# Optimization experiments

Measured on AMD Instinct MI355X. Metric: run time of the kernel, lower is better.

The kernel has to match this reference:

```python
import jax, jax.numpy as jnp
import numpy as np

N_NODES = 100000  # static segment count for segment_sum
DEGREE = 2        # polynomial degree of the Laplacian filter


def setup_inputs() -> dict:
    key = jax.random.key(0)
    k1, k2, k3, k4 = jax.random.split(key, 4)
    N, E, C = N_NODES, 1600000, 32
    x = jax.random.normal(k1, (N, C), dtype=jnp.float32)
    weights = jax.random.normal(k2, (1 + DEGREE,), dtype=jnp.float32)
    edge_src = jax.random.randint(k3, (E,), 0, N, dtype=jnp.int32)
    edge_dst = jax.random.randint(k4, (E,), 0, N, dtype=jnp.int32)
    return {"x": x, "weights": weights, "edge_src": edge_src, "edge_dst": edge_dst}


def reference(x, weights, edge_src, edge_dst):
    """y = (w0 * I + w1 * L + ... + w_d * L^d) @ x with L = D - A,
    computed by the recurrence t_k = L @ t_{k-1} (never materializing L^k)."""
    N = N_NODES
    # node degrees: D[i] = number of edges landing on i
    deg = jax.ops.segment_sum(jnp.ones_like(edge_src, dtype=x.dtype), edge_dst,
                              num_segments=N)  # [N]

    def lap_matvec(t):
        # (L @ t)[i] = deg[i] * t[i] - sum_{(s->i) in E} t[s]
        agg = jax.ops.segment_sum(t[edge_src], edge_dst, num_segments=N)  # [N, C]
        return deg[:, None] * t - agg

    y = weights[0] * x
    t = x
    for k in range(1, 1 + DEGREE):  # fixed small loop over polynomial order
        t = lap_matvec(t)
        y = y + weights[k] * t
    return y
```

## Files before the change

kernel.cpp:

```cpp
#include <hip/hip_runtime.h>

#define C 32
#define NT 256
#define BSH 8
#define BNODE 256
#define CAPC 5632
#define SRCMASK 0x1FFFF

typedef float f32x4 __attribute__((ext_vector_type(4)));

__device__ __forceinline__ unsigned int f2bf(float f) {
    unsigned int u = __float_as_uint(f);
    return (u + 0x7FFFu + ((u >> 16) & 1u)) >> 16;
}
__device__ __forceinline__ float bflo(unsigned int u) { return __uint_as_float(u << 16); }
__device__ __forceinline__ float bfhi(unsigned int u) { return __uint_as_float(u & 0xFFFF0000u); }

__global__ __launch_bounds__(1024) void phaseA(const int* __restrict__ src,
                                               const int* __restrict__ dst,
                                               int* __restrict__ cursor,
                                               int* __restrict__ pk,
                                               int E, int nbuck, int chunk) {
    extern __shared__ int l[];
    int* lcnt = l;
    int* lcur = l + nbuck;
    int tid = threadIdx.x;
    for (int i = tid; i < nbuck; i += 1024) lcnt[i] = 0;
    __syncthreads();
    int base = blockIdx.x * chunk;
    int end  = min(base + chunk, E);
    for (int e = base + tid; e < end; e += 1024)
        atomicAdd(&lcnt[dst[e] >> BSH], 1);
    __syncthreads();
    for (int i = tid; i < nbuck; i += 1024) {
        int c = lcnt[i];
        lcur[i] = i * CAPC + (c ? atomicAdd(&cursor[i], c) : 0);
    }
    __syncthreads();
    for (int e = base + tid; e < end; e += 1024) {
        int d = dst[e];
        int b = d >> BSH;
        int pos = atomicAdd(&lcur[b], 1);
        pk[pos] = src[e] | ((d & (BNODE - 1)) << 17);
    }
}

__global__ __launch_bounds__(1024) void phaseB(int* __restrict__ pk,
                                               const int* __restrict__ cursor,
                                               int* __restrict__ row_start,
                                               int* __restrict__ ideg,
                                               const float* __restrict__ x,
                                               uint2* __restrict__ xb2, int N) {
    __shared__ int ent[CAPC];
    __shared__ int h[BNODE];
    __shared__ int ss[BNODE];
    __shared__ int cur[BNODE];
    int b = blockIdx.x;
    int tid = threadIdx.x;

    if (tid < BNODE) h[tid] = 0;

    int n0 = b << BSH;
    int nvalid = min(N - n0, BNODE);
    for (int i = tid; i < nvalid * 8; i += 1024) {
        int n = n0 + (i >> 3);
        int lq = i & 7;
        const float* xp = x + (size_t)n * C + lq * 4;
        uint2 r;
        r.x = f2bf(xp[0]) | (f2bf(xp[1]) << 16);
        r.y = f2bf(xp[2]) | (f2bf(xp[3]) << 16);
        xb2[(size_t)n * 8 + lq] = r;
    }

    int base = b * CAPC;
    int cnt = min(cursor[b], CAPC);
    __syncthreads();
    for (int i = tid; i < cnt; i += 1024) {
        int en = pk[base + i];
        ent[i] = en;
        atomicAdd(&h[en >> 17], 1);
    }
    __syncthreads();
    int v = 0;
    if (tid < BNODE) { v = h[tid]; ss[tid] = v; }
    __syncthreads();
    for (int off = 1; off < BNODE; off <<= 1) {
        int u = 0;
        if (tid < BNODE && tid >= off) u = ss[tid - off];
        __syncthreads();
        if (tid < BNODE) ss[tid] += u;
        __syncthreads();
    }
    if (tid < BNODE) {
        int exc = ss[tid] - v;
        int n = n0 + tid;
        if (n < N) { row_start[n] = base + exc; ideg[n] = v; }
        cur[tid] = exc;
    }
    __syncthreads();
    for (int i = tid; i < cnt; i += 1024) {
        int en = ent[i];
        int pos = atomicAdd(&cur[en >> 17], 1);
        pk[base + pos] = en & SRCMASK;
    }
}

__device__ __forceinline__ void accum_seg(const uint2* __restrict__ arr,
                                          const int* __restrict__ pk,
                                          int lo, int hi, int lq,
                                          float& a0, float& a1, float& a2, float& a3) {
#define ACC4(ux, uy) { a0 += bflo(ux); a1 += bfhi(ux); a2 += bflo(uy); a3 += bfhi(uy); }
    int j = lo;
    for (; j + 7 < hi; j += 8) {
        int s0 = __builtin_nontemporal_load(&pk[j]);
        int s1 = __builtin_nontemporal_load(&pk[j + 1]);
        int s2 = __builtin_nontemporal_load(&pk[j + 2]);
        int s3 = __builtin_nontemporal_load(&pk[j + 3]);
        int s4 = __builtin_nontemporal_load(&pk[j + 4]);
        int s5 = __builtin_nontemporal_load(&pk[j + 5]);
        int s6 = __builtin_nontemporal_load(&pk[j + 6]);
        int s7 = __builtin_nontemporal_load(&pk[j + 7]);
        uint2 u0 = arr[(size_t)s0 * 8 + lq];
        uint2 u1 = arr[(size_t)s1 * 8 + lq];
        uint2 u2 = arr[(size_t)s2 * 8 + lq];
        uint2 u3 = arr[(size_t)s3 * 8 + lq];
        uint2 u4 = arr[(size_t)s4 * 8 + lq];
        uint2 u5 = arr[(size_t)s5 * 8 + lq];
        uint2 u6 = arr[(size_t)s6 * 8 + lq];
        uint2 u7 = arr[(size_t)s7 * 8 + lq];
        ACC4(u0.x, u0.y) ACC4(u1.x, u1.y) ACC4(u2.x, u2.y) ACC4(u3.x, u3.y)
        ACC4(u4.x, u4.y) ACC4(u5.x, u5.y) ACC4(u6.x, u6.y) ACC4(u7.x, u7.y)
    }
    for (; j + 1 < hi; j += 2) {
        int s0 = __builtin_nontemporal_load(&pk[j]);
        int s1 = __builtin_nontemporal_load(&pk[j + 1]);
        uint2 u0 = arr[(size_t)s0 * 8 + lq];
        uint2 u1 = arr[(size_t)s1 * 8 + lq];
        ACC4(u0.x, u0.y) ACC4(u1.x, u1.y)
    }
    if (j < hi) {
        uint2 u0 = arr[(size_t)__builtin_nontemporal_load(&pk[j]) * 8 + lq];
        ACC4(u0.x, u0.y)
    }
#undef ACC4
}

__global__ __launch_bounds__(NT) void gather1_bf(const uint2* __restrict__ xb2,
        const int* __restrict__ pk, const int* __restrict__ row_start,
        const int* __restrict__ ideg, uint2* __restrict__ t1b2, int N) {
    int g = blockIdx.x * blockDim.x + threadIdx.x;
    int n = g >> 3;
    if (n >= N) return;
    int lq = g & 7;
    int rs = row_start[n];
    int dg = ideg[n];
    float a0 = 0.f, a1 = 0.f, a2 = 0.f, a3 = 0.f;
    accum_seg(xb2, pk, rs, rs + dg, lq, a0, a1, a2, a3);
    uint2 xs = xb2[(size_t)n * 8 + lq];
    float fdg = (float)dg;
    float t0 = fdg * bflo(xs.x) - a0;
    float t1v = fdg * bfhi(xs.x) - a1;
    float t2 = fdg * bflo(xs.y) - a2;
    float t3 = fdg * bfhi(xs.y) - a3;
    uint2 r;
    r.x = f2bf(t0) | (f2bf(t1v) << 16);
    r.y = f2bf(t2) | (f2bf(t3) << 16);
    t1b2[(size_t)n * 8 + lq] = r;
}

__global__ __launch_bounds__(NT) void gather2_bf(const uint2* __restrict__ xb2,
        const uint2* __restrict__ t1b2, const int* __restrict__ pk,
        const int* __restrict__ row_start, const int* __restrict__ ideg,
        const float* __restrict__ wts, float* __restrict__ y, int N) {
    int g = blockIdx.x * blockDim.x + threadIdx.x;
    int n = g >> 3;
    if (n >= N) return;
    int lq = g & 7;
    int rs = row_start[n];
    int dg = ideg[n];
    float a0 = 0.f, a1 = 0.f, a2 = 0.f, a3 = 0.f;
    accum_seg(t1b2, pk, rs, rs + dg, lq, a0, a1, a2, a3);
    uint2 xs = xb2[(size_t)n * 8 + lq];
    uint2 ts = t1b2[(size_t)n * 8 + lq];
    float w0 = wts[0], w1 = wts[1], w2 = wts[2];
    float fdg = (float)dg;
    float tv0 = bflo(ts.x), tv1 = bfhi(ts.x), tv2 = bflo(ts.y), tv3 = bfhi(ts.y);
    f32x4 r;
    r.x = w0 * bflo(xs.x) + w1 * tv0 + w2 * (fdg * tv0 - a0);
    r.y = w0 * bfhi(xs.x) + w1 * tv1 + w2 * (fdg * tv1 - a1);
    r.z = w0 * bflo(xs.y) + w1 * tv2 + w2 * (fdg * tv2 - a2);
    r.w = w0 * bfhi(xs.y) + w1 * tv3 + w2 * (fdg * tv3 - a3);
    size_t o = (size_t)n * C + lq * 4;
    __builtin_nontemporal_store(r, (f32x4*)(y + o));
}

__global__ __launch_bounds__(NT) void gather1_f32(const float* __restrict__ x,
        const int* __restrict__ pk, const int* __restrict__ row_start,
        const int* __restrict__ ideg, float* __restrict__ t1, int N) {
    int g = blockIdx.x * blockDim.x + threadIdx.x;
    int n = g >> 5;
    if (n >= N) return;
    int ch = g & 31;
    int rs = row_start[n], dg = ideg[n], re = rs + dg;
    float a0 = 0, a1 = 0, a2 = 0, a3 = 0;
    int j = rs;
    for (; j + 3 < re; j += 4) {
        a0 += x[(size_t)pk[j] * C + ch];     a1 += x[(size_t)pk[j + 1] * C + ch];
        a2 += x[(size_t)pk[j + 2] * C + ch]; a3 += x[(size_t)pk[j + 3] * C + ch];
    }
    for (; j < re; ++j) a0 += x[(size_t)pk[j] * C + ch];
    size_t o = (size_t)n * C + ch;
    t1[o] = (float)dg * x[o] - ((a0 + a1) + (a2 + a3));
}
__global__ __launch_bounds__(NT) void gather2_f32(const float* __restrict__ x,
        const float* __restrict__ t1, const int* __restrict__ pk,
        const int* __restrict__ row_start, const int* __restrict__ ideg,
        const float* __restrict__ wts, float* __restrict__ y, int N) {
    int g = blockIdx.x * blockDim.x + threadIdx.x;
    int n = g >> 5;
    if (n >= N) return;
    int ch = g & 31;
    int rs = row_start[n], dg = ideg[n], re = rs + dg;
    float a0 = 0, a1 = 0, a2 = 0, a3 = 0;
    int j = rs;
    for (; j + 3 < re; j += 4) {
        a0 += t1[(size_t)pk[j] * C + ch];     a1 += t1[(size_t)pk[j + 1] * C + ch];
        a2 += t1[(size_t)pk[j + 2] * C + ch]; a3 += t1[(size_t)pk[j + 3] * C + ch];
    }
    for (; j < re; ++j) a0 += t1[(size_t)pk[j] * C + ch];
    size_t o = (size_t)n * C + ch;
    float tv = t1[o];
    y[o] = wts[0] * x[o] + wts[1] * tv + wts[2] * ((float)dg * tv - ((a0 + a1) + (a2 + a3)));
}

extern "C" void kernel_launch(void* const* d_in, const int* in_sizes, int n_in,
                              void* d_out, int out_size, void* d_ws, size_t ws_size,
                              hipStream_t stream) {
    const float* x    = (const float*)d_in[0];
    const float* wts  = (const float*)d_in[1];
    const int*   esrc = (const int*)d_in[2];
    const int*   edst = (const int*)d_in[3];
    float*       y    = (float*)d_out;

    const int N = in_sizes[0] / C;
    const int E = in_sizes[2];
    const int nbuck = (N + BNODE - 1) >> BSH;
    const int nc = N * C;

    char* p = (char*)d_ws;
    auto align16 = [](size_t s) { return (s + 15) & ~(size_t)15; };
    int* cursor    = (int*)p; p += align16((size_t)nbuck * 4);
    int* row_start = (int*)p; p += align16((size_t)N * 4);
    int* ideg      = (int*)p; p += align16((size_t)N * 4);
    int* pk        = (int*)p; p += align16((size_t)nbuck * CAPC * 4);
    uint2* xb2     = (uint2*)p; p += align16((size_t)nc * 2);
    uint2* t1b2    = (uint2*)p; p += align16((size_t)nc * 2);
    float* t1      = (float*)p;
    bool bf_ok = (size_t)(p - (char*)d_ws) <= ws_size;

    hipMemsetAsync(cursor, 0, (size_t)nbuck * 4, stream);

    const int ABLK = 512;
    const int chunk = (E + ABLK - 1) / ABLK;
    const size_t lds_a = (size_t)nbuck * 2 * 4;
    phaseA<<<ABLK, 1024, lds_a, stream>>>(esrc, edst, cursor, pk, E, nbuck, chunk);
    phaseB<<<nbuck, 1024, 0, stream>>>(pk, cursor, row_start, ideg, x, xb2, N);

    if (bf_ok) {
        const int gblocks = ((size_t)N * 8 + NT - 1) / NT;
        gather1_bf<<<gblocks, NT, 0, stream>>>(xb2, pk, row_start, ideg, t1b2, N);
        gather2_bf<<<gblocks, NT, 0, stream>>>(xb2, t1b2, pk, row_start, ideg, wts, y, N);
    } else {
        const int gblocks = ((size_t)N * 32 + NT - 1) / NT;
        gather1_f32<<<gblocks, NT, 0, stream>>>(x, pk, row_start, ideg, t1, N);
        gather2_f32<<<gblocks, NT, 0, stream>>>(x, t1, pk, row_start, ideg, wts, y, N);
    }
}
```

Before: 174.7 us.

## Split bf16 feature arrays into two channel halves and gather each half separately

Stores the bf16 copies of x and t1 as two separate 16-channel planes and runs each gather pass twice, once per half. Each half-plane is 3.2 MB instead of 6.4 MB, so the random gathers are meant to fit better in cache and get a higher hit rate. The cost is reading the CSR index array twice per pass and launching more kernels, and each gathered row now covers 32 bytes instead of 64. It also switches the t1 stores to nontemporal stores.

```diff
diff --git a/kernel.cpp b/kernel.cpp
--- a/kernel.cpp
+++ b/kernel.cpp
@@ -50,7 +50,8 @@
                                                int* __restrict__ row_start,
                                                int* __restrict__ ideg,
                                                const float* __restrict__ x,
-                                               uint2* __restrict__ xb2, int N) {
+                                               uint2* __restrict__ xbh,
+                                               int N) {
     __shared__ int ent[CAPC];
     __shared__ int h[BNODE];
     __shared__ int ss[BNODE];
@@ -62,14 +63,17 @@
 
     int n0 = b << BSH;
     int nvalid = min(N - n0, BNODE);
-    for (int i = tid; i < nvalid * 8; i += 1024) {
-        int n = n0 + (i >> 3);
-        int lq = i & 7;
-        const float* xp = x + (size_t)n * C + lq * 4;
-        uint2 r;
-        r.x = f2bf(xp[0]) | (f2bf(xp[1]) << 16);
-        r.y = f2bf(xp[2]) | (f2bf(xp[3]) << 16);
-        xb2[(size_t)n * 8 + lq] = r;
+    size_t N4 = (size_t)N * 4;
+    for (int hh = 0; hh < 2; ++hh) {
+        for (int i = tid; i < nvalid * 4; i += 1024) {
+            int n = n0 + (i >> 2);
+            int lq2 = i & 3;
+            const float* xp = x + (size_t)n * C + hh * 16 + lq2 * 4;
+            uint2 r;
+            r.x = f2bf(xp[0]) | (f2bf(xp[1]) << 16);
+            r.y = f2bf(xp[2]) | (f2bf(xp[3]) << 16);
+            xbh[hh * N4 + (size_t)n * 4 + lq2] = r;
+        }
     }
 
     int base = b * CAPC;
@@ -105,10 +109,10 @@
     }
 }
 
-__device__ __forceinline__ void accum_seg(const uint2* __restrict__ arr,
-                                          const int* __restrict__ pk,
-                                          int lo, int hi, int lq,
-                                          float& a0, float& a1, float& a2, float& a3) {
+__device__ __forceinline__ void accum_half(const uint2* __restrict__ arr,
+                                           const int* __restrict__ pk,
+                                           int lo, int hi, int lq2,
+                                           float& a0, float& a1, float& a2, float& a3) {
 #define ACC4(ux, uy) { a0 += bflo(ux); a1 += bfhi(ux); a2 += bflo(uy); a3 += bfhi(uy); }
     int j = lo;
     for (; j + 7 < hi; j += 8) {
@@ -120,43 +124,43 @@
         int s5 = __builtin_nontemporal_load(&pk[j + 5]);
         int s6 = __builtin_nontemporal_load(&pk[j + 6]);
         int s7 = __builtin_nontemporal_load(&pk[j + 7]);
-        uint2 u0 = arr[(size_t)s0 * 8 + lq];
-        uint2 u1 = arr[(size_t)s1 * 8 + lq];
-        uint2 u2 = arr[(size_t)s2 * 8 + lq];
-        uint2 u3 = arr[(size_t)s3 * 8 + lq];
-        uint2 u4 = arr[(size_t)s4 * 8 + lq];
-        uint2 u5 = arr[(size_t)s5 * 8 + lq];
-        uint2 u6 = arr[(size_t)s6 * 8 + lq];
-        uint2 u7 = arr[(size_t)s7 * 8 + lq];
+        uint2 u0 = arr[(size_t)s0 * 4 + lq2];
+        uint2 u1 = arr[(size_t)s1 * 4 + lq2];
+        uint2 u2 = arr[(size_t)s2 * 4 + lq2];
+        uint2 u3 = arr[(size_t)s3 * 4 + lq2];
+        uint2 u4 = arr[(size_t)s4 * 4 + lq2];
+        uint2 u5 = arr[(size_t)s5 * 4 + lq2];
+        uint2 u6 = arr[(size_t)s6 * 4 + lq2];
+        uint2 u7 = arr[(size_t)s7 * 4 + lq2];
         ACC4(u0.x, u0.y) ACC4(u1.x, u1.y) ACC4(u2.x, u2.y) ACC4(u3.x, u3.y)
         ACC4(u4.x, u4.y) ACC4(u5.x, u5.y) ACC4(u6.x, u6.y) ACC4(u7.x, u7.y)
     }
     for (; j + 1 < hi; j += 2) {
         int s0 = __builtin_nontemporal_load(&pk[j]);
         int s1 = __builtin_nontemporal_load(&pk[j + 1]);
-        uint2 u0 = arr[(size_t)s0 * 8 + lq];
-        uint2 u1 = arr[(size_t)s1 * 8 + lq];
+        uint2 u0 = arr[(size_t)s0 * 4 + lq2];
+        uint2 u1 = arr[(size_t)s1 * 4 + lq2];
         ACC4(u0.x, u0.y) ACC4(u1.x, u1.y)
     }
     if (j < hi) {
-        uint2 u0 = arr[(size_t)__builtin_nontemporal_load(&pk[j]) * 8 + lq];
+        uint2 u0 = arr[(size_t)__builtin_nontemporal_load(&pk[j]) * 4 + lq2];
         ACC4(u0.x, u0.y)
     }
 #undef ACC4
 }
 
-__global__ __launch_bounds__(NT) void gather1_bf(const uint2* __restrict__ xb2,
+__global__ __launch_bounds__(NT) void gather1_half(const uint2* __restrict__ xh,
         const int* __restrict__ pk, const int* __restrict__ row_start,
-        const int* __restrict__ ideg, uint2* __restrict__ t1b2, int N) {
-    int g = blockIdx.x * blockDim.x + threadIdx.x;
-    int n = g >> 3;
-    if (n >= N) return;
-    int lq = g & 7;
+        const int* __restrict__ ideg, uint2* __restrict__ t1h, int N) {
+    int g = blockIdx.x * blockDim.x + threadIdx.x;
+    int n = g >> 2;
+    if (n >= N) return;
+    int lq2 = g & 3;
     int rs = row_start[n];
     int dg = ideg[n];
     float a0 = 0.f, a1 = 0.f, a2 = 0.f, a3 = 0.f;
-    accum_seg(xb2, pk, rs, rs + dg, lq, a0, a1, a2, a3);
-    uint2 xs = xb2[(size_t)n * 8 + lq];
+    accum_half(xh, pk, rs, rs + dg, lq2, a0, a1, a2, a3);
+    uint2 xs = xh[(size_t)n * 4 + lq2];
     float fdg = (float)dg;
     float t0 = fdg * bflo(xs.x) - a0;
     float t1v = fdg * bfhi(xs.x) - a1;
@@ -165,23 +169,24 @@
     uint2 r;
     r.x = f2bf(t0) | (f2bf(t1v) << 16);
     r.y = f2bf(t2) | (f2bf(t3) << 16);
-    t1b2[(size_t)n * 8 + lq] = r;
-}
-
-__global__ __launch_bounds__(NT) void gather2_bf(const uint2* __restrict__ xb2,
-        const uint2* __restrict__ t1b2, const int* __restrict__ pk,
+    __builtin_nontemporal_store(r.x, &((unsigned int*)t1h)[((size_t)n * 4 + lq2) * 2]);
+    __builtin_nontemporal_store(r.y, &((unsigned int*)t1h)[((size_t)n * 4 + lq2) * 2 + 1]);
+}
+
+__global__ __launch_bounds__(NT) void gather2_half(const uint2* __restrict__ xh,
+        const uint2* __restrict__ t1h, const int* __restrict__ pk,
         const int* __restrict__ row_start, const int* __restrict__ ideg,
-        const float* __restrict__ wts, float* __restrict__ y, int N) {
-    int g = blockIdx.x * blockDim.x + threadIdx.x;
-    int n = g >> 3;
-    if (n >= N) return;
-    int lq = g & 7;
+        const float* __restrict__ wts, float* __restrict__ y, int N, int hh) {
+    int g = blockIdx.x * blockDim.x + threadIdx.x;
+    int n = g >> 2;
+    if (n >= N) return;
+    int lq2 = g & 3;
     int rs = row_start[n];
     int dg = ideg[n];
     float a0 = 0.f, a1 = 0.f, a2 = 0.f, a3 = 0.f;
-    accum_seg(t1b2, pk, rs, rs + dg, lq, a0, a1, a2, a3);
-    uint2 xs = xb2[(size_t)n * 8 + lq];
-    uint2 ts = t1b2[(size_t)n * 8 + lq];
+    accum_half(t1h, pk, rs, rs + dg, lq2, a0, a1, a2, a3);
+    uint2 xs = xh[(size_t)n * 4 + lq2];
+    uint2 ts = t1h[(size_t)n * 4 + lq2];
     float w0 = wts[0], w1 = wts[1], w2 = wts[2];
     float fdg = (float)dg;
     float tv0 = bflo(ts.x), tv1 = bfhi(ts.x), tv2 = bflo(ts.y), tv3 = bfhi(ts.y);
@@ -190,7 +195,7 @@
     r.y = w0 * bfhi(xs.x) + w1 * tv1 + w2 * (fdg * tv1 - a1);
     r.z = w0 * bflo(xs.y) + w1 * tv2 + w2 * (fdg * tv2 - a2);
     r.w = w0 * bfhi(xs.y) + w1 * tv3 + w2 * (fdg * tv3 - a3);
-    size_t o = (size_t)n * C + lq * 4;
+    size_t o = (size_t)n * C + hh * 16 + lq2 * 4;
     __builtin_nontemporal_store(r, (f32x4*)(y + o));
 }
 
@@ -246,6 +251,7 @@
     const int E = in_sizes[2];
     const int nbuck = (N + BNODE - 1) >> BSH;
     const int nc = N * C;
+    const size_t N4 = (size_t)N * 4;
 
     char* p = (char*)d_ws;
     auto align16 = [](size_t s) { return (s + 15) & ~(size_t)15; };
@@ -253,9 +259,9 @@
     int* row_start = (int*)p; p += align16((size_t)N * 4);
     int* ideg      = (int*)p; p += align16((size_t)N * 4);
     int* pk        = (int*)p; p += align16((size_t)nbuck * CAPC * 4);
-    uint2* xb2     = (uint2*)p; p += align16((size_t)nc * 2);
-    uint2* t1b2    = (uint2*)p; p += align16((size_t)nc * 2);
-    float* t1      = (float*)p;
+    uint2* xbh     = (uint2*)p; p += align16(N4 * 2 * 8);
+    uint2* t1bh    = (uint2*)p; p += align16(N4 * 2 * 8);
+    float* t1      = (float*)p; p += align16((size_t)nc * 4);
     bool bf_ok = (size_t)(p - (char*)d_ws) <= ws_size;
 
     hipMemsetAsync(cursor, 0, (size_t)nbuck * 4, stream);
@@ -264,12 +270,14 @@
     const int chunk = (E + ABLK - 1) / ABLK;
     const size_t lds_a = (size_t)nbuck * 2 * 4;
     phaseA<<<ABLK, 1024, lds_a, stream>>>(esrc, edst, cursor, pk, E, nbuck, chunk);
-    phaseB<<<nbuck, 1024, 0, stream>>>(pk, cursor, row_start, ideg, x, xb2, N);
+    phaseB<<<nbuck, 1024, 0, stream>>>(pk, cursor, row_start, ideg, x, xbh, N);
 
     if (bf_ok) {
-        const int gblocks = ((size_t)N * 8 + NT - 1) / NT;
-        gather1_bf<<<gblocks, NT, 0, stream>>>(xb2, pk, row_start, ideg, t1b2, N);
-        gather2_bf<<<gblocks, NT, 0, stream>>>(xb2, t1b2, pk, row_start, ideg, wts, y, N);
+        const int gblocks = ((size_t)N * 4 + NT - 1) / NT;
+        gather1_half<<<gblocks, NT, 0, stream>>>(xbh,      pk, row_start, ideg, t1bh,      N);
+        gather1_half<<<gblocks, NT, 0, stream>>>(xbh + N4, pk, row_start, ideg, t1bh + N4, N);
+        gather2_half<<<gblocks, NT, 0, stream>>>(xbh,      t1bh,      pk, row_start, ideg, wts, y, N, 0);
+        gather2_half<<<gblocks, NT, 0, stream>>>(xbh + N4, t1bh + N4, pk, row_start, ideg, wts, y, N, 1);
     } else {
         const int gblocks = ((size_t)N * 32 + NT - 1) / NT;
         gather1_f32<<<gblocks, NT, 0, stream>>>(x, pk, row_start, ideg, t1, N);
```

Measured after the change: 201.4 us. 1.15x slower.

## Fuse first Laplacian matvec into bucket sort and bf16 convert into phaseA

Applied to the files above, without the earlier changes.

Moves the fp32-to-bf16 conversion of x into the edge-scatter kernel as a grid-stride tail loop. The first Laplacian pass is fused into the per-bucket sort kernel, reading sorted source indices from LDS instead of reloading pk from global memory. This drops the separate gather1 launch and one pass over the index array. In exchange, each bucket block now does the gather work with only 391 blocks of 1024 threads, which may reduce latency hiding, and the sort kernel needs extra LDS. A dead stub remains in the old phaseA.

```diff
diff --git a/kernel.cpp b/kernel.cpp
--- a/kernel.cpp
+++ b/kernel.cpp
@@ -20,7 +20,8 @@
                                                const int* __restrict__ dst,
                                                int* __restrict__ cursor,
                                                int* __restrict__ pk,
-                                               int E, int nbuck, int chunk) {
+                                               uint2* __restrict__ xb2,
+                                               int N, int E, int nbuck, int chunk) {
     extern __shared__ int l[];
     int* lcnt = l;
     int* lcur = l + nbuck;
@@ -43,37 +44,72 @@
         int pos = atomicAdd(&lcur[b], 1);
         pk[pos] = src[e] | ((d & (BNODE - 1)) << 17);
     }
-}
-
-__global__ __launch_bounds__(1024) void phaseB(int* __restrict__ pk,
-                                               const int* __restrict__ cursor,
-                                               int* __restrict__ row_start,
-                                               int* __restrict__ ideg,
-                                               const float* __restrict__ x,
-                                               uint2* __restrict__ xb2, int N) {
+    if (xb2 != nullptr) {
+        const float* xf = (const float*)dst;
+    }
+}
+
+__global__ __launch_bounds__(1024) void phaseA_cvt(const int* __restrict__ src,
+                                                   const int* __restrict__ dst,
+                                                   int* __restrict__ cursor,
+                                                   int* __restrict__ pk,
+                                                   const float* __restrict__ x,
+                                                   uint2* __restrict__ xb2,
+                                                   int N, int E, int nbuck, int chunk) {
+    extern __shared__ int l[];
+    int* lcnt = l;
+    int* lcur = l + nbuck;
+    int tid = threadIdx.x;
+    for (int i = tid; i < nbuck; i += 1024) lcnt[i] = 0;
+    __syncthreads();
+    int base = blockIdx.x * chunk;
+    int end  = min(base + chunk, E);
+    for (int e = base + tid; e < end; e += 1024)
+        atomicAdd(&lcnt[dst[e] >> BSH], 1);
+    __syncthreads();
+    for (int i = tid; i < nbuck; i += 1024) {
+        int c = lcnt[i];
+        lcur[i] = i * CAPC + (c ? atomicAdd(&cursor[i], c) : 0);
+    }
+    __syncthreads();
+    for (int e = base + tid; e < end; e += 1024) {
+        int d = dst[e];
+        int b = d >> BSH;
+        int pos = atomicAdd(&lcur[b], 1);
+        pk[pos] = src[e] | ((d & (BNODE - 1)) << 17);
+    }
+    if (xb2 != nullptr) {
+        int total = N * 8;
+        int gid = blockIdx.x * 1024 + tid;
+        int gth = gridDim.x * 1024;
+        for (int i = gid; i < total; i += gth) {
+            f32x4 v = *(const f32x4*)(x + (size_t)i * 4);
+            uint2 r;
+            r.x = f2bf(v.x) | (f2bf(v.y) << 16);
+            r.y = f2bf(v.z) | (f2bf(v.w) << 16);
+            xb2[i] = r;
+        }
+    }
+}
+
+__global__ __launch_bounds__(1024) void phaseB_mv1(int* __restrict__ pk,
+                                                   const int* __restrict__ cursor,
+                                                   int* __restrict__ row_start,
+                                                   int* __restrict__ ideg,
+                                                   const uint2* __restrict__ xb2,
+                                                   uint2* __restrict__ t1b2, int N) {
     __shared__ int ent[CAPC];
+    __shared__ int sorted[CAPC];
     __shared__ int h[BNODE];
     __shared__ int ss[BNODE];
     __shared__ int cur[BNODE];
     int b = blockIdx.x;
     int tid = threadIdx.x;
-
-    if (tid < BNODE) h[tid] = 0;
-
     int n0 = b << BSH;
-    int nvalid = min(N - n0, BNODE);
-    for (int i = tid; i < nvalid * 8; i += 1024) {
-        int n = n0 + (i >> 3);
-        int lq = i & 7;
-        const float* xp = x + (size_t)n * C + lq * 4;
-        uint2 r;
-        r.x = f2bf(xp[0]) | (f2bf(xp[1]) << 16);
-        r.y = f2bf(xp[2]) | (f2bf(xp[3]) << 16);
-        xb2[(size_t)n * 8 + lq] = r;
-    }
-
     int base = b * CAPC;
     int cnt = min(cursor[b], CAPC);
+
+    if (tid < BNODE) h[tid] = 0;
     __syncthreads();
     for (int i = tid; i < cnt; i += 1024) {
         int en = pk[base + i];
@@ -101,7 +137,47 @@
     for (int i = tid; i < cnt; i += 1024) {
         int en = ent[i];
         int pos = atomicAdd(&cur[en >> 17], 1);
-        pk[base + pos] = en & SRCMASK;
+        int s = en & SRCMASK;
+        sorted[pos] = s;
+        pk[base + pos] = s;
+    }
+    __syncthreads();
+
+    for (int i = tid; i < BNODE * 8; i += 1024) {
+        int r = i >> 3;
+        int lq = i & 7;
+        int n = n0 + r;
+        if (n >= N) continue;
+        int hi = ss[r];
+        int lo = hi - h[r];
+        float a0 = 0.f, a1 = 0.f, a2 = 0.f, a3 = 0.f;
+        int j = lo;
+        for (; j + 3 < hi; j += 4) {
+            int s0 = sorted[j], s1 = sorted[j + 1], s2 = sorted[j + 2], s3 = sorted[j + 3];
+            uint2 u0 = xb2[(size_t)s0 * 8 + lq];
+            uint2 u1 = xb2[(size_t)s1 * 8 + lq];
+            uint2 u2 = xb2[(size_t)s2 * 8 + lq];
+            uint2 u3 = xb2[(size_t)s3 * 8 + lq];
+            a0 += bflo(u0.x); a1 += bfhi(u0.x); a2 += bflo(u0.y); a3 += bfhi(u0.y);
+            a0 += bflo(u1.x); a1 += bfhi(u1.x); a2 += bflo(u1.y); a3 += bfhi(u1.y);
+            a0 += bflo(u2.x); a1 += bfhi(u2.x); a2 += bflo(u2.y); a3 += bfhi(u2.y);
+            a0 += bflo(u3.x); a1 += bfhi(u3.x); a2 += bflo(u3.y); a3 += bfhi(u3.y);
+        }
+        for (; j < hi; ++j) {
+            uint2 u0 = xb2[(size_t)sorted[j] * 8 + lq];
+            a0 += bflo(u0.x); a1 += bfhi(u0.x); a2 += bflo(u0.y); a3 += bfhi(u0.y);
+        }
+        uint2 xs = xb2[(size_t)n * 8 + lq];
+        float fdg = (float)h[r];
+        float t0 = fdg * bflo(xs.x) - a0;
+        float t1v = fdg * bfhi(xs.x) - a1;
+        float t2 = fdg * bflo(xs.y) - a2;
+        float t3 = fdg * bfhi(xs.y) - a3;
+        uint2 rr;
+        rr.x = f2bf(t0) | (f2bf(t1v) << 16);
+        rr.y = f2bf(t2) | (f2bf(t3) << 16);
+        __builtin_nontemporal_store(rr.x, &((unsigned int*)t1b2)[((size_t)n * 8 + lq) * 2]);
+        __builtin_nontemporal_store(rr.y, &((unsigned int*)t1b2)[((size_t)n * 8 + lq) * 2 + 1]);
     }
 }
 
@@ -145,29 +221,6 @@
 #undef ACC4
 }
 
-__global__ __launch_bounds__(NT) void gather1_bf(const uint2* __restrict__ xb2,
-        const int* __restrict__ pk, const int* __restrict__ row_start,
-        const int* __restrict__ ideg, uint2* __restrict__ t1b2, int N) {
-    int g = blockIdx.x * blockDim.x + threadIdx.x;
-    int n = g >> 3;
-    if (n >= N) return;
-    int lq = g & 7;
-    int rs = row_start[n];
-    int dg = ideg[n];
-    float a0 = 0.f, a1 = 0.f, a2 = 0.f, a3 = 0.f;
-    accum_seg(xb2, pk, rs, rs + dg, lq, a0, a1, a2, a3);
-    uint2 xs = xb2[(size_t)n * 8 + lq];
-    float fdg = (float)dg;
-    float t0 = fdg * bflo(xs.x) - a0;
-    float t1v = fdg * bfhi(xs.x) - a1;
-    float t2 = fdg * bflo(xs.y) - a2;
-    float t3 = fdg * bfhi(xs.y) - a3;
-    uint2 r;
-    r.x = f2bf(t0) | (f2bf(t1v) << 16);
-    r.y = f2bf(t2) | (f2bf(t3) << 16);
-    t1b2[(size_t)n * 8 + lq] = r;
-}
-
 __global__ __launch_bounds__(NT) void gather2_bf(const uint2* __restrict__ xb2,
         const uint2* __restrict__ t1b2, const int* __restrict__ pk,
         const int* __restrict__ row_start, const int* __restrict__ ideg,
@@ -194,6 +247,48 @@
     __builtin_nontemporal_store(r, (f32x4*)(y + o));
 }
 
+__global__ __launch_bounds__(1024) void phaseB_sort(int* __restrict__ pk,
+        const int* __restrict__ cursor, int* __restrict__ row_start,
+        int* __restrict__ ideg, int N) {
+    __shared__ int ent[CAPC];
+    __shared__ int h[BNODE];
+    __shared__ int ss[BNODE];
+    __shared__ int cur[BNODE];
+    int b = blockIdx.x;
+    int tid = threadIdx.x;
+    int base = b * CAPC;
+    int cnt = min(cursor[b], CAPC);
+    if (tid < BNODE) h[tid] = 0;
+    __syncthreads();
+    for (int i = tid; i < cnt; i += 1024) {
+        int en = pk[base + i];
+        ent[i] = en;
+        atomicAdd(&h[en >> 17], 1);
+    }
+    __syncthreads();
+    int v = 0;
+    if (tid < BNODE) { v = h[tid]; ss[tid] = v; }
+    __syncthreads();
+    for (int off = 1; off < BNODE; off <<= 1) {
+        int u = 0;
+        if (tid < BNODE && tid >= off) u = ss[tid - off];
+        __syncthreads();
+        if (tid < BNODE) ss[tid] += u;
+        __syncthreads();
+    }
+    if (tid < BNODE) {
+        int exc = ss[tid] - v;
+        int n = (b << BSH) + tid;
+        if (n < N) { row_start[n] = base + exc; ideg[n] = v; }
+        cur[tid] = exc;
+    }
+    __syncthreads();
+    for (int i = tid; i < cnt; i += 1024) {
+        int en = ent[i];
+        int pos = atomicAdd(&cur[en >> 17], 1);
+        pk[base + pos] = en & SRCMASK;
+    }
+}
 __global__ __launch_bounds__(NT) void gather1_f32(const float* __restrict__ x,
         const int* __restrict__ pk, const int* __restrict__ row_start,
         const int* __restrict__ ideg, float* __restrict__ t1, int N) {
@@ -263,14 +358,18 @@
     const int ABLK = 512;
     const int chunk = (E + ABLK - 1) / ABLK;
     const size_t lds_a = (size_t)nbuck * 2 * 4;
-    phaseA<<<ABLK, 1024, lds_a, stream>>>(esrc, edst, cursor, pk, E, nbuck, chunk);
-    phaseB<<<nbuck, 1024, 0, stream>>>(pk, cursor, row_start, ideg, x, xb2, N);
 
     if (bf_ok) {
+        phaseA_cvt<<<ABLK, 1024, lds_a, stream>>>(esrc, edst, cursor, pk, x, xb2,
+                                                  N, E, nbuck, chunk);
+        phaseB_mv1<<<nbuck, 1024, 0, stream>>>(pk, cursor, row_start, ideg,
+                                               xb2, t1b2, N);
         const int gblocks = ((size_t)N * 8 + NT - 1) / NT;
-        gather1_bf<<<gblocks, NT, 0, stream>>>(xb2, pk, row_start, ideg, t1b2, N);
         gather2_bf<<<gblocks, NT, 0, stream>>>(xb2, t1b2, pk, row_start, ideg, wts, y, N);
     } else {
+        phaseA_cvt<<<ABLK, 1024, lds_a, stream>>>(esrc, edst, cursor, pk, x, nullptr,
+                                                  N, E, nbuck, chunk);
+        phaseB_sort<<<nbuck, 1024, 0, stream>>>(pk, cursor, row_start, ideg, N);
         const int gblocks = ((size_t)N * 32 + NT - 1) / NT;
         gather1_f32<<<gblocks, NT, 0, stream>>>(x, pk, row_start, ideg, t1, N);
         gather2_f32<<<gblocks, NT, 0, stream>>>(x, t1, pk, row_start, ideg, wts, y, N);
```

After: 169.6 us. 2.9% less time.
